# Performance work log

Measured on AMD Instinct MI355X. Metric: run time of the kernel, lower is better.

The kernel has to match this reference:

```python
import jax, jax.numpy as jnp
import numpy as np

EMPTY = -1  # sentinel for empty (vertex, region) slots, as in the TF layer


def setup_inputs() -> dict:
    key = jax.random.key(0)
    m, vertices, regions = 128, 2048, 32
    # values in [-1, vertices): -1 marks an empty slot, otherwise a vertex id
    mapping = jax.random.randint(key, (m, vertices, regions), EMPTY, vertices, dtype=jnp.int32)
    return {"mapping": mapping}


def reference(mapping):
    """Faithful JAX version of Graph2Col.call.

    TF's tf.where(mask) emits coordinates of True entries in row-major order
    with a data-dependent row count. For jit-compatibility we emit a
    fixed-size [m*V*R, ...] result where valid entries come first (same
    row-major order as tf.where) and padding rows are filled with -1.
    """
    m, V, R = mapping.shape
    total = m * V * R
    flat_map = mapping.reshape(-1)                 # [total]
    # row index is never -1, so the reduce_all mask is simply mapping != -1
    flat_mask = flat_map != EMPTY                  # [total] bool

    # stable stream compaction: valid entries first, preserving row-major order
    order = jnp.argsort(~flat_mask)                # stable sort -> tf.where ordering
    valid = flat_mask[order]                       # [total] bool

    rows = order // (V * R)
    rem = order % (V * R)
    verts = rem // R
    regs = rem % R

    # column_indices: coordinates of non-empty slots (tf.where returns int64)
    column_indices = jnp.stack([rows, verts, regs], axis=-1).astype(jnp.int64)  # [total, 3]
    # nodes_indices: (batch_row, vertex_id) gathered at those coordinates (int32)
    nodes_indices = jnp.stack([rows.astype(jnp.int32), flat_map[order]], axis=-1)  # [total, 2]

    column_indices = jnp.where(valid[:, None], column_indices, jnp.int64(EMPTY))
    nodes_indices = jnp.where(valid[:, None], nodes_indices, jnp.int32(EMPTY))
    return nodes_indices, column_indices
```

## Files before the change

kernel.cpp:

```cpp
#include <hip/hip_runtime.h>


#define EMPTY_V (-1)

typedef int v4i __attribute__((ext_vector_type(4)));

constexpr int TOTAL = 8388608;
constexpr int BLOCK = 256;
constexpr int CHUNK = 4096;
constexpr int NB = TOTAL / CHUNK;
constexpr int SUBT = CHUNK / (BLOCK * 4);
constexpr int NWAVE = BLOCK / 64;

__device__ __forceinline__ int SW(int i) { return i ^ ((i >> 5) & 3); }

__global__ __launch_bounds__(BLOCK) void k_count(const int* __restrict__ in,
                                                 int* __restrict__ counts) {
    const int b = blockIdx.x;
    const int tid = threadIdx.x;
    const int4* p = (const int4*)(in + (size_t)b * CHUNK);
    int c = 0;
#pragma unroll
    for (int s = 0; s < SUBT; ++s) {
        int4 v = p[s * BLOCK + tid];
        c += (v.x != EMPTY_V) + (v.y != EMPTY_V) + (v.z != EMPTY_V) + (v.w != EMPTY_V);
    }
    for (int d = 32; d; d >>= 1) c += __shfl_down(c, d, 64);
    __shared__ int ws[NWAVE];
    const int lane = tid & 63, wid = tid >> 6;
    if (lane == 0) ws[wid] = c;
    __syncthreads();
    if (tid == 0) counts[b] = ws[0] + ws[1] + ws[2] + ws[3];
}

__global__ __launch_bounds__(BLOCK) void k_scatter(const int* __restrict__ in,
                                                   const int* __restrict__ counts,
                                                   int* __restrict__ out_nodes,
                                                   int* __restrict__ out_cols) {
    const int b = blockIdx.x;
    const int tid = threadIdx.x;
    const int lane = tid & 63, wid = tid >> 6;
    const unsigned long long below = lane ? ((~0ull) >> (64 - lane)) : 0ull;

    __shared__ int red[NWAVE], redt[NWAVE];
    __shared__ int wsum[SUBT * NWAVE];
    __shared__ int s_val[CHUNK];
    __shared__ int s_pos[CHUNK];

    {
        const int4 ca = ((const int4*)counts)[2 * tid];
        const int4 cb = ((const int4*)counts)[2 * tid + 1];
        const int idx0 = tid * 8;
        const int cs[8] = {ca.x, ca.y, ca.z, ca.w, cb.x, cb.y, cb.z, cb.w};
        int pa = 0, ta = 0;
#pragma unroll
        for (int j = 0; j < 8; ++j) {
            ta += cs[j];
            if (idx0 + j < b) pa += cs[j];
        }
        for (int d = 32; d; d >>= 1) {
            pa += __shfl_down(pa, d, 64);
            ta += __shfl_down(ta, d, 64);
        }
        if (lane == 0) { red[wid] = pa; redt[wid] = ta; }
    }

    int4 v[SUBT];
    int pre[SUBT];
    const int4* p = (const int4*)(in + (size_t)b * CHUNK);
#pragma unroll
    for (int s = 0; s < SUBT; ++s) {
        v[s] = p[s * BLOCK + tid];
        const unsigned long long b0 = __ballot(v[s].x != EMPTY_V);
        const unsigned long long b1 = __ballot(v[s].y != EMPTY_V);
        const unsigned long long b2 = __ballot(v[s].z != EMPTY_V);
        const unsigned long long b3 = __ballot(v[s].w != EMPTY_V);
        pre[s] = __popcll(b0 & below) + __popcll(b1 & below) +
                 __popcll(b2 & below) + __popcll(b3 & below);
        if (lane == 0)
            wsum[s * NWAVE + wid] =
                __popcll(b0) + __popcll(b1) + __popcll(b2) + __popcll(b3);
    }
    __syncthreads();

    const int excl = red[0] + red[1] + red[2] + red[3];
    int myoff[SUBT];
    int acc = 0;
#pragma unroll
    for (int s = 0; s < SUBT; ++s) {
        int cs_ = 0, woff = 0;
#pragma unroll
        for (int w = 0; w < NWAVE; ++w) {
            const int x = wsum[s * NWAVE + w];
            cs_ += x;
            if (w < wid) woff += x;
        }
        myoff[s] = acc + woff + pre[s];
        acc += cs_;
    }
    const int blockValid = acc;

#pragma unroll
    for (int s = 0; s < SUBT; ++s) {
        int lp = myoff[s];
        const int rem0 = ((b & 15) << 12) + (s << 10) + (tid << 2);
        const int vals[4] = {v[s].x, v[s].y, v[s].z, v[s].w};
#pragma unroll
        for (int j = 0; j < 4; ++j) {
            if (vals[j] != EMPTY_V) {
                s_val[SW(lp)] = vals[j];
                s_pos[SW(lp)] = rem0 + j;
                ++lp;
            }
        }
    }
    __syncthreads();

    const int row = b >> 4;
    const int cnt = blockValid;

    {
        int2* b2p = (int2*)out_nodes + excl;
        const int head = ((excl & 1) && cnt > 0) ? 1 : 0;
        if (head && tid == 0) b2p[0] = make_int2(row, s_val[SW(0)]);
        const int nPairs = (cnt - head) >> 1;
        v4i* b4p = (v4i*)(b2p + head);
        for (int k = tid; k < nPairs; k += BLOCK) {
            const int e = head + 2 * k;
            v4i t = {row, s_val[SW(e)], row, s_val[SW(e + 1)]};
            __builtin_nontemporal_store(t, &b4p[k]);
        }
        if (((cnt - head) & 1) && tid == BLOCK - 1)
            b2p[cnt - 1] = make_int2(row, s_val[SW(cnt - 1)]);
    }
    {
        int* cd = out_cols + 3 * (size_t)excl;
        const int cdw = 3 * cnt;
        const int mis = (3 * excl) & 3;
        int peel = mis ? (4 - mis) : 0;
        if (peel > cdw) peel = cdw;
        if (tid < peel) {
            const int ld = tid;
            const int e = ld / 3, r = ld - 3 * e;
            int vv = row;
            if (r) { const int pp = s_pos[SW(e)]; vv = (r == 1) ? (pp >> 5) : (pp & 31); }
            cd[ld] = vv;
        }
        const int body = (cdw - peel) >> 2;
        v4i* c4p = (v4i*)(cd + peel);
        for (int k = tid; k < body; k += BLOCK) {
            const int ld0 = peel + 4 * k;
            int vv[4];
#pragma unroll
            for (int i = 0; i < 4; ++i) {
                const int ld = ld0 + i;
                const int e = ld / 3, r = ld - 3 * e;
                int x = row;
                if (r) { const int pp = s_pos[SW(e)]; x = (r == 1) ? (pp >> 5) : (pp & 31); }
                vv[i] = x;
            }
            v4i t = {vv[0], vv[1], vv[2], vv[3]};
            __builtin_nontemporal_store(t, &c4p[k]);
        }
        const int tails = cdw - peel - 4 * body;
        if (tid < tails) {
            const int ld = peel + 4 * body + tid;
            const int e = ld / 3, r = ld - 3 * e;
            int vv = row;
            if (r) { const int pp = s_pos[SW(e)]; vv = (r == 1) ? (pp >> 5) : (pp & 31); }
            cd[ld] = vv;
        }
    }

    {
        const int inv_pref = b * CHUNK - excl;
        const int start = TOTAL - inv_pref - (CHUNK - blockValid);
        const int end = TOTAL - inv_pref;
        for (int pos = start + tid; pos < end; pos += BLOCK) {
            out_nodes[2 * pos]     = EMPTY_V;
            out_nodes[2 * pos + 1] = EMPTY_V;
            out_cols[3 * pos]      = EMPTY_V;
            out_cols[3 * pos + 1]  = EMPTY_V;
            out_cols[3 * pos + 2]  = EMPTY_V;
        }
    }
}

extern "C" void kernel_launch(void* const* d_in, const int* in_sizes, int n_in,
                              void* d_out, int out_size, void* d_ws, size_t ws_size,
                              hipStream_t stream) {
    const int* in = (const int*)d_in[0];
    int* out = (int*)d_out;
    int* out_nodes = out;
    int* out_cols = out + 2 * (size_t)TOTAL;
    int* counts = (int*)d_ws;

    k_count<<<NB, BLOCK, 0, stream>>>(in, counts);
    k_scatter<<<NB, BLOCK, 0, stream>>>(in, counts, out_nodes, out_cols);
}
```

Measured before the change: 200.9 us.

## Stage fully interleaved output rows in LDS and halve chunk size

The chunk size drops from 4096 to 2048 elements, which doubles the block count and changes the row/remainder arithmetic to match. Compacted entries are now written into LDS already laid out as the final nodes (2-int) and cols (3-int) records, so a generic aligned vector copy can stream them out and the per-element divide-by-3 is gone. The XOR swizzle and nontemporal stores are dropped, and the count prefix now reads 16 counts per thread. The interleaved stride-2 and stride-3 LDS writes may cause bank conflicts, and the larger count table means more prefix work per block.

```diff
diff --git a/kernel.cpp b/kernel.cpp
--- a/kernel.cpp
+++ b/kernel.cpp
@@ -7,12 +7,10 @@
 
 constexpr int TOTAL = 8388608;
 constexpr int BLOCK = 256;
-constexpr int CHUNK = 4096;
+constexpr int CHUNK = 2048;
 constexpr int NB = TOTAL / CHUNK;
 constexpr int SUBT = CHUNK / (BLOCK * 4);
 constexpr int NWAVE = BLOCK / 64;
-
-__device__ __forceinline__ int SW(int i) { return i ^ ((i >> 5) & 3); }
 
 __global__ __launch_bounds__(BLOCK) void k_count(const int* __restrict__ in,
                                                  int* __restrict__ counts) {
@@ -33,6 +31,27 @@
     if (tid == 0) counts[b] = ws[0] + ws[1] + ws[2] + ws[3];
 }
 
+__device__ __forceinline__ void copy_out(int* __restrict__ dst,
+                                         const int* __restrict__ src,
+                                         int ndw, int tid) {
+    const int mis = (int)(((uintptr_t)dst >> 2) & 3);
+    int peel = mis ? (4 - mis) : 0;
+    if (peel > ndw) peel = ndw;
+    if (tid < peel) dst[tid] = src[tid];
+    const int body = (ndw - peel) >> 2;
+    v4i* d4 = (v4i*)(dst + peel);
+    const int* s4 = src + peel;
+    for (int k = tid; k < body; k += BLOCK) {
+        v4i t = {s4[4 * k], s4[4 * k + 1], s4[4 * k + 2], s4[4 * k + 3]};
+        d4[k] = t;
+    }
+    const int tails = ndw - peel - 4 * body;
+    if (tid < tails) {
+        const int ld = peel + 4 * body + tid;
+        dst[ld] = src[ld];
+    }
+}
+
 __global__ __launch_bounds__(BLOCK) void k_scatter(const int* __restrict__ in,
                                                    const int* __restrict__ counts,
                                                    int* __restrict__ out_nodes,
@@ -42,27 +61,24 @@
     const int lane = tid & 63, wid = tid >> 6;
     const unsigned long long below = lane ? ((~0ull) >> (64 - lane)) : 0ull;
 
-    __shared__ int red[NWAVE], redt[NWAVE];
-    __shared__ int wsum[SUBT * NWAVE];
-    __shared__ int s_val[CHUNK];
-    __shared__ int s_pos[CHUNK];
+    __shared__ int s_nodes[2 * CHUNK];
+    __shared__ int s_cols[3 * CHUNK];
+    int* RED = s_nodes;
+    int* WSUM = s_nodes + NWAVE;
 
     {
-        const int4 ca = ((const int4*)counts)[2 * tid];
-        const int4 cb = ((const int4*)counts)[2 * tid + 1];
-        const int idx0 = tid * 8;
-        const int cs[8] = {ca.x, ca.y, ca.z, ca.w, cb.x, cb.y, cb.z, cb.w};
-        int pa = 0, ta = 0;
+        int pa = 0;
+        const int idx0 = tid * 16;
 #pragma unroll
-        for (int j = 0; j < 8; ++j) {
-            ta += cs[j];
-            if (idx0 + j < b) pa += cs[j];
+        for (int q = 0; q < 4; ++q) {
+            const int4 c4 = ((const int4*)counts)[4 * tid + q];
+            const int cs[4] = {c4.x, c4.y, c4.z, c4.w};
+#pragma unroll
+            for (int j = 0; j < 4; ++j)
+                if (idx0 + 4 * q + j < b) pa += cs[j];
         }
-        for (int d = 32; d; d >>= 1) {
-            pa += __shfl_down(pa, d, 64);
-            ta += __shfl_down(ta, d, 64);
-        }
-        if (lane == 0) { red[wid] = pa; redt[wid] = ta; }
+        for (int d = 32; d; d >>= 1) pa += __shfl_down(pa, d, 64);
+        if (lane == 0) RED[wid] = pa;
     }
 
     int4 v[SUBT];
@@ -78,12 +94,12 @@
         pre[s] = __popcll(b0 & below) + __popcll(b1 & below) +
                  __popcll(b2 & below) + __popcll(b3 & below);
         if (lane == 0)
-            wsum[s * NWAVE + wid] =
+            WSUM[s * NWAVE + wid] =
                 __popcll(b0) + __popcll(b1) + __popcll(b2) + __popcll(b3);
     }
     __syncthreads();
 
-    const int excl = red[0] + red[1] + red[2] + red[3];
+    const int excl = RED[0] + RED[1] + RED[2] + RED[3];
     int myoff[SUBT];
     int acc = 0;
 #pragma unroll
@@ -91,7 +107,7 @@
         int cs_ = 0, woff = 0;
 #pragma unroll
         for (int w = 0; w < NWAVE; ++w) {
-            const int x = wsum[s * NWAVE + w];
+            const int x = WSUM[s * NWAVE + w];
             cs_ += x;
             if (w < wid) woff += x;
         }
@@ -99,78 +115,31 @@
         acc += cs_;
     }
     const int blockValid = acc;
+    __syncthreads();
 
+    const int row = b >> 5;
 #pragma unroll
     for (int s = 0; s < SUBT; ++s) {
         int lp = myoff[s];
-        const int rem0 = ((b & 15) << 12) + (s << 10) + (tid << 2);
+        const int rem0 = ((b & 31) << 11) + (s << 10) + (tid << 2);
         const int vals[4] = {v[s].x, v[s].y, v[s].z, v[s].w};
 #pragma unroll
         for (int j = 0; j < 4; ++j) {
             if (vals[j] != EMPTY_V) {
-                s_val[SW(lp)] = vals[j];
-                s_pos[SW(lp)] = rem0 + j;
+                const int pp = rem0 + j;
+                s_nodes[2 * lp] = row;
+                s_nodes[2 * lp + 1] = vals[j];
+                s_cols[3 * lp] = row;
+                s_cols[3 * lp + 1] = pp >> 5;
+                s_cols[3 * lp + 2] = pp & 31;
                 ++lp;
             }
         }
     }
     __syncthreads();
 
-    const int row = b >> 4;
-    const int cnt = blockValid;
-
-    {
-        int2* b2p = (int2*)out_nodes + excl;
-        const int head = ((excl & 1) && cnt > 0) ? 1 : 0;
-        if (head && tid == 0) b2p[0] = make_int2(row, s_val[SW(0)]);
-        const int nPairs = (cnt - head) >> 1;
-        v4i* b4p = (v4i*)(b2p + head);
-        for (int k = tid; k < nPairs; k += BLOCK) {
-            const int e = head + 2 * k;
-            v4i t = {row, s_val[SW(e)], row, s_val[SW(e + 1)]};
-            __builtin_nontemporal_store(t, &b4p[k]);
-        }
-        if (((cnt - head) & 1) && tid == BLOCK - 1)
-            b2p[cnt - 1] = make_int2(row, s_val[SW(cnt - 1)]);
-    }
-    {
-        int* cd = out_cols + 3 * (size_t)excl;
-        const int cdw = 3 * cnt;
-        const int mis = (3 * excl) & 3;
-        int peel = mis ? (4 - mis) : 0;
-        if (peel > cdw) peel = cdw;
-        if (tid < peel) {
-            const int ld = tid;
-            const int e = ld / 3, r = ld - 3 * e;
-            int vv = row;
-            if (r) { const int pp = s_pos[SW(e)]; vv = (r == 1) ? (pp >> 5) : (pp & 31); }
-            cd[ld] = vv;
-        }
-        const int body = (cdw - peel) >> 2;
-        v4i* c4p = (v4i*)(cd + peel);
-        for (int k = tid; k < body; k += BLOCK) {
-            const int ld0 = peel + 4 * k;
-            int vv[4];
-#pragma unroll
-            for (int i = 0; i < 4; ++i) {
-                const int ld = ld0 + i;
-                const int e = ld / 3, r = ld - 3 * e;
-                int x = row;
-                if (r) { const int pp = s_pos[SW(e)]; x = (r == 1) ? (pp >> 5) : (pp & 31); }
-                vv[i] = x;
-            }
-            v4i t = {vv[0], vv[1], vv[2], vv[3]};
-            __builtin_nontemporal_store(t, &c4p[k]);
-        }
-        const int tails = cdw - peel - 4 * body;
-        if (tid < tails) {
-            const int ld = peel + 4 * body + tid;
-            const int e = ld / 3, r = ld - 3 * e;
-            int vv = row;
-            if (r) { const int pp = s_pos[SW(e)]; vv = (r == 1) ? (pp >> 5) : (pp & 31); }
-            cd[ld] = vv;
-        }
-    }
+    copy_out(out_nodes + 2 * (size_t)excl, s_nodes, 2 * blockValid, tid);
+    copy_out(out_cols + 3 * (size_t)excl, s_cols, 3 * blockValid, tid);
 
     {
         const int inv_pref = b * CHUNK - excl;
```

Measured after the change: 189.4 us, median of 2. 1.06x faster.
